# Performance work log

Measured on AMD Instinct MI355X. Metric: run time of the kernel, lower is better.

Reference implementation:

```python
import jax, jax.numpy as jnp
import numpy as np

B, S, N, D, H, M, P_OFF = 16, 4, 2048, 128, 16, 4096, 4092


def setup_inputs() -> dict:
    key = jax.random.key(0)
    ks = jax.random.split(key, 6)
    return {
        "X": jax.random.normal(ks[0], (B, S, N), dtype=jnp.float32),
        "W_q": jax.random.normal(ks[1], (N, N), dtype=jnp.float32) * 0.02,
        "W_k": jax.random.normal(ks[2], (N, N), dtype=jnp.float32) * 0.02,
        "W_v": jax.random.normal(ks[3], (N, N), dtype=jnp.float32) * 0.02,
        "cache_K": jax.random.normal(ks[4], (B, H, M, D), dtype=jnp.float32),
        "cache_V": jax.random.normal(ks[5], (B, H, M, D), dtype=jnp.float32),
        "P": P_OFF,
    }


def reference(X, W_q, W_k, W_v, cache_K, cache_V, P):
    b, s, n = X.shape
    _, h, m, d = cache_K.shape
    # RMSNorm (no eps, no learned scale, matching the source)
    variance = jnp.mean(X * X, axis=-1, keepdims=True)
    X_norm = X * jax.lax.rsqrt(variance)
    # QKV projections -> [b, h, s, d]
    Q = (X_norm @ W_q).reshape(b, s, h, d).transpose(0, 2, 1, 3)
    K = (X_norm @ W_k).reshape(b, s, h, d).transpose(0, 2, 1, 3)
    V = (X_norm @ W_v).reshape(b, s, h, d).transpose(0, 2, 1, 3)
    # KV-cache write at static offset P
    cK = cache_K.at[:, :, P:P + s, :].set(K)
    cV = cache_V.at[:, :, P:P + s, :].set(V)
    # Attention over full cache (note: source applies no 1/sqrt(d) scale)
    scores = jnp.einsum("bhsd,bhmd->bhsm", Q, cK)
    attn = jax.nn.softmax(scores, axis=-1)
    O = jnp.einsum("bhsm,bhmd->bhsd", attn, cV)
    return O.transpose(0, 2, 1, 3).reshape(b, s, n)
```

## Files before the change

### kernel.cpp

```cpp
#include <hip/hip_runtime.h>
#include <hip/hip_bf16.h>
#include <math.h>

#define NB 16
#define NS 4
#define NN 2048
#define ND 128
#define NH 16
#define NM 4096
#define NCHK 8
#define CHROWS 512
#define TROWS 32
#define NT 16
#define NKC 16

#define XN_OFF   0u
#define Q_OFF    131072u
#define K_OFF    262144u
#define V_OFF    393216u
#define OP_OFF   524288u
#define ML_OFF   1572864u
#define PART_OFF 1589248u

__global__ __launch_bounds__(256) void k_rmsnorm(const float* __restrict__ X,
                                                 float* __restrict__ ws) {
    const int row = blockIdx.x;
    const int tid = threadIdx.x;
    const float* xr = X + (size_t)row * NN;
    float4 a = *(const float4*)(xr + tid * 4);
    float4 b = *(const float4*)(xr + 1024 + tid * 4);
    float ss = a.x*a.x + a.y*a.y + a.z*a.z + a.w*a.w
             + b.x*b.x + b.y*b.y + b.z*b.z + b.w*b.w;
    #pragma unroll
    for (int off = 32; off; off >>= 1) ss += __shfl_xor(ss, off);
    __shared__ float ls[4];
    if ((tid & 63) == 0) ls[tid >> 6] = ss;
    __syncthreads();
    const float r = rsqrtf((ls[0] + ls[1] + ls[2] + ls[3]) * (1.0f / NN));
    float* o = ws + XN_OFF + (size_t)row * NN;
    *(float4*)(o + tid * 4)        = make_float4(a.x*r, a.y*r, a.z*r, a.w*r);
    *(float4*)(o + 1024 + tid * 4) = make_float4(b.x*r, b.y*r, b.z*r, b.w*r);
}

__global__ __launch_bounds__(256) void k_qkv(const float* __restrict__ Wq,
                                             const float* __restrict__ Wk,
                                             const float* __restrict__ Wv,
                                             float* __restrict__ ws) {
    __shared__ float xsT[64][68];
    __shared__ float wt[64][132];
    const int ct    = blockIdx.x;
    const int which = blockIdx.y;
    const int kc    = blockIdx.z;
    const float* __restrict__ W = (which == 0) ? Wq : (which == 1) ? Wk : Wv;
    const int tid = threadIdx.x;
    const int c0  = ct * 128;
    const int rg  = tid >> 5;
    const int cg  = tid & 31;
    const float* xn = ws + XN_OFF;

    float4 acc[8];
    #pragma unroll
    for (int i = 0; i < 8; i++) acc[i] = make_float4(0.f, 0.f, 0.f, 0.f);

    for (int s = 0; s < 2; s++) {
        const int k0 = kc * 128 + s * 64;
        __syncthreads();
        {
            const int r  = tid >> 2;
            const int q4 = tid & 3;
            #pragma unroll
            for (int i = 0; i < 4; i++) {
                const int f4 = q4 + i * 4;
                float4 v = *(const float4*)(xn + (size_t)r * NN + k0 + f4 * 4);
                xsT[f4 * 4 + 0][r] = v.x;
                xsT[f4 * 4 + 1][r] = v.y;
                xsT[f4 * 4 + 2][r] = v.z;
                xsT[f4 * 4 + 3][r] = v.w;
            }
        }
        {
            #pragma unroll
            for (int j8 = 0; j8 < 8; j8++) {
                const int kk  = j8 * 8 + (tid >> 5);
                const int f4c = tid & 31;
                float4 v = *(const float4*)(W + (size_t)(k0 + kk) * NN + c0 + f4c * 4);
                *(float4*)&wt[kk][f4c * 4] = v;
            }
        }
        __syncthreads();
        #pragma unroll 8
        for (int kk = 0; kk < 64; kk++) {
            const float4 x0 = *(const float4*)&xsT[kk][rg * 8];
            const float4 x1 = *(const float4*)&xsT[kk][rg * 8 + 4];
            const float4 w4 = *(const float4*)&wt[kk][cg * 4];
            acc[0].x += x0.x*w4.x; acc[0].y += x0.x*w4.y; acc[0].z += x0.x*w4.z; acc[0].w += x0.x*w4.w;
            acc[1].x += x0.y*w4.x; acc[1].y += x0.y*w4.y; acc[1].z += x0.y*w4.z; acc[1].w += x0.y*w4.w;
            acc[2].x += x0.z*w4.x; acc[2].y += x0.z*w4.y; acc[2].z += x0.z*w4.z; acc[2].w += x0.z*w4.w;
            acc[3].x += x0.w*w4.x; acc[3].y += x0.w*w4.y; acc[3].z += x0.w*w4.z; acc[3].w += x0.w*w4.w;
            acc[4].x += x1.x*w4.x; acc[4].y += x1.x*w4.y; acc[4].z += x1.x*w4.z; acc[4].w += x1.x*w4.w;
            acc[5].x += x1.y*w4.x; acc[5].y += x1.y*w4.y; acc[5].z += x1.y*w4.z; acc[5].w += x1.y*w4.w;
            acc[6].x += x1.z*w4.x; acc[6].y += x1.z*w4.y; acc[6].z += x1.z*w4.z; acc[6].w += x1.z*w4.w;
            acc[7].x += x1.w*w4.x; acc[7].y += x1.w*w4.y; acc[7].z += x1.w*w4.z; acc[7].w += x1.w*w4.w;
        }
    }
    float* po = ws + PART_OFF + (size_t)(kc * 3 + which) * 131072u;
    #pragma unroll
    for (int i = 0; i < 8; i++)
        *(float4*)(po + (size_t)(rg * 8 + i) * NN + c0 + cg * 4) = acc[i];
}

__global__ __launch_bounds__(256) void k_reduce(float* __restrict__ ws) {
    const int idx = blockIdx.x * 256 + threadIdx.x;
    const int which = idx >> 15;
    const int off   = idx & 32767;
    float4 s = make_float4(0.f, 0.f, 0.f, 0.f);
    #pragma unroll
    for (int kcc = 0; kcc < NKC; kcc++) {
        const float4 v = *(const float4*)(ws + PART_OFF
                         + (size_t)(kcc * 3 + which) * 131072u + (size_t)off * 4);
        s.x += v.x; s.y += v.y; s.z += v.z; s.w += v.w;
    }
    *(float4*)(ws + Q_OFF + (size_t)which * 131072u + (size_t)off * 4) = s;
}

__global__ __launch_bounds__(256) void k_attn(const float* __restrict__ cK,
                                              const float* __restrict__ cV,
                                              const int* __restrict__ Pp,
                                              float* __restrict__ ws) {
    const int ch = blockIdx.x, h = blockIdx.y, b = blockIdx.z;
    const int tid = threadIdx.x;
    const int wv = tid >> 6, lane = tid & 63;
    const int half = lane >> 5, r32 = lane & 31;
    const int P = *Pp;
    __shared__ float Ks[2][TROWS * 128];
    __shared__ float Vs[2][TROWS * 128];
    __shared__ float Qs[4][128] __attribute__((aligned(16)));
    __shared__ float ps[TROWS][4] __attribute__((aligned(16)));
    __shared__ float facs[4] __attribute__((aligned(16)));
    __shared__ float Ow[4][4][128];
    __shared__ float mls[4][2];

    if (tid < 128) {
        const int q = tid >> 5, d = (tid & 31) * 4;
        *(float4*)&Qs[q][d] =
            *(const float4*)(ws + Q_OFF + (size_t)(b * 4 + q) * NN + h * 128 + d);
    }

    const float* kbase = cK + (size_t)(b * NH + h) * NM * ND;
    const float* vbase = cV + (size_t)(b * NH + h) * NM * ND;
    const float* knew  = ws + K_OFF;
    const float* vnew  = ws + V_OFF;
    const int mb0 = ch * CHROWS;

    auto STAGE = [&](int tt, int bufi) {
        const int mb = mb0 + tt * TROWS;
        #pragma unroll
        for (int i = 0; i < 4; i++) {
            const int g0  = (wv * 4 + i) * 64;
            const int g   = g0 + lane;
            const int row = g >> 5;
            const int c4  = g & 31;
            const int csw = c4 ^ (row & 7);
            const int mrow = mb + row;
            const float* src = (mrow >= P && mrow < P + NS)
                ? knew + (size_t)(b * 4 + (mrow - P)) * NN + h * 128 + csw * 4
                : kbase + (size_t)mrow * ND + csw * 4;
            __builtin_amdgcn_global_load_lds(
                (const __attribute__((address_space(1))) void*)src,
                (__attribute__((address_space(3))) void*)(&Ks[bufi][g0 * 4]),
                16, 0, 0);
        }
        #pragma unroll
        for (int i = 0; i < 4; i++) {
            const int g0  = (wv * 4 + i) * 64;
            const int g   = g0 + lane;
            const int row = g >> 5;
            const int c4  = g & 31;
            const int mrow = mb + row;
            const float* src = (mrow >= P && mrow < P + NS)
                ? vnew + (size_t)(b * 4 + (mrow - P)) * NN + h * 128 + c4 * 4
                : vbase + (size_t)mrow * ND + c4 * 4;
            __builtin_amdgcn_global_load_lds(
                (const __attribute__((address_space(1))) void*)src,
                (__attribute__((address_space(3))) void*)(&Vs[bufi][g0 * 4]),
                16, 0, 0);
        }
    };

    float m_run = -INFINITY, l_run = 0.f;
    float2 Oa[4];
    #pragma unroll
    for (int q = 0; q < 4; q++) Oa[q] = make_float2(0.f, 0.f);

    STAGE(0, 0);
    __syncthreads();

    for (int t = 0; t < NT; t++) {
        const int cur = t & 1;
        if (t < NT - 1) STAGE(t + 1, cur ^ 1);

        const int s7 = r32 & 7;
        const float* kr = &Ks[cur][r32 * 128 + half * 64];
        const float* qr = &Qs[wv][half * 64];
        float s = 0.f;
        #pragma unroll
        for (int j = 0; j < 16; j++) {
            const float4 k4 = *(const float4*)&kr[(j ^ s7) * 4];
            const float4 q4 = *(const float4*)&qr[j * 4];
            s += k4.x*q4.x + k4.y*q4.y + k4.z*q4.z + k4.w*q4.w;
        }
        s += __shfl_xor(s, 32);
        float wm = s;
        #pragma unroll
        for (int off = 16; off; off >>= 1) wm = fmaxf(wm, __shfl_xor(wm, off));
        const float mn  = fmaxf(m_run, wm);
        const float fac = __expf(m_run - mn);
        m_run = mn;
        const float p = __expf(s - mn);
        l_run = l_run * fac + ((half == 0) ? p : 0.f);
        if (half == 0) ps[r32][wv] = p;
        if (lane == 0) facs[wv] = fac;
        asm volatile("s_waitcnt lgkmcnt(0)" ::: "memory");
        __builtin_amdgcn_s_barrier();
        __builtin_amdgcn_sched_barrier(0);

        const float4 fq = *(const float4*)&facs[0];
        Oa[0].x *= fq.x; Oa[0].y *= fq.x;
        Oa[1].x *= fq.y; Oa[1].y *= fq.y;
        Oa[2].x *= fq.z; Oa[2].y *= fq.z;
        Oa[3].x *= fq.w; Oa[3].y *= fq.w;
        const int r0 = wv * 8;
        #pragma unroll
        for (int rr = 0; rr < 8; rr++) {
            const float2 v2 = *(const float2*)&Vs[cur][(r0 + rr) * 128 + lane * 2];
            const float4 pr = *(const float4*)&ps[r0 + rr][0];
            Oa[0].x += pr.x * v2.x; Oa[0].y += pr.x * v2.y;
            Oa[1].x += pr.y * v2.x; Oa[1].y += pr.y * v2.y;
            Oa[2].x += pr.z * v2.x; Oa[2].y += pr.z * v2.y;
            Oa[3].x += pr.w * v2.x; Oa[3].y += pr.w * v2.y;
        }
        __syncthreads();
    }

    #pragma unroll
    for (int off = 32; off; off >>= 1) l_run += __shfl_xor(l_run, off);
    #pragma unroll
    for (int q = 0; q < 4; q++)
        *(float2*)&Ow[wv][q][lane * 2] = Oa[q];
    if (lane == 0) { mls[wv][0] = m_run; mls[wv][1] = l_run; }
    __syncthreads();

    const int q = wv;
    const int d0 = lane * 2;
    float o0 = 0.f, o1 = 0.f;
    #pragma unroll
    for (int w2 = 0; w2 < 4; w2++) {
        o0 += Ow[w2][q][d0];
        o1 += Ow[w2][q][d0 + 1];
    }
    const size_t bh = (size_t)(b * NH + h);
    const size_t pidx = ((bh * NCHK + ch) * 4 + q) * 128 + d0;
    ws[OP_OFF + pidx]     = o0;
    ws[OP_OFF + pidx + 1] = o1;
    if (lane == 0) {
        const size_t mi = ((bh * NCHK + ch) * 4 + q) * 2;
        ws[ML_OFF + mi]     = mls[q][0];
        ws[ML_OFF + mi + 1] = mls[q][1];
    }
}

__global__ __launch_bounds__(256) void k_comb(const float* __restrict__ ws,
                                              float* __restrict__ out) {
    const int bh = blockIdx.x;
    const int b = bh >> 4, h = bh & 15;
    const int tid = threadIdx.x;
    const int q = tid >> 6, d0 = (tid & 63) * 2;
    float ms = -INFINITY;
    #pragma unroll
    for (int c = 0; c < NCHK; c++)
        ms = fmaxf(ms, ws[ML_OFF + (((size_t)bh * NCHK + c) * 4 + q) * 2]);
    float o0 = 0.f, o1 = 0.f, den = 0.f;
    #pragma unroll
    for (int c = 0; c < NCHK; c++) {
        const size_t mi = (((size_t)bh * NCHK + c) * 4 + q) * 2;
        float e = __expf(ws[ML_OFF + mi] - ms);
        den += e * ws[ML_OFF + mi + 1];
        const size_t pi = (((size_t)bh * NCHK + c) * 4 + q) * 128 + d0;
        o0 += e * ws[OP_OFF + pi];
        o1 += e * ws[OP_OFF + pi + 1];
    }
    const float inv = 1.0f / den;
    const size_t oi = (size_t)(b * 4 + q) * NN + h * 128 + d0;
    *(float2*)(out + oi) = make_float2(o0 * inv, o1 * inv);
}

extern "C" void kernel_launch(void* const* d_in, const int* in_sizes, int n_in,
                              void* d_out, int out_size, void* d_ws, size_t ws_size,
                              hipStream_t stream) {
    const float* X  = (const float*)d_in[0];
    const float* Wq = (const float*)d_in[1];
    const float* Wk = (const float*)d_in[2];
    const float* Wv = (const float*)d_in[3];
    const float* cK = (const float*)d_in[4];
    const float* cV = (const float*)d_in[5];
    const int*   Pp = (const int*)d_in[6];
    float* ws = (float*)d_ws;
    float* out = (float*)d_out;

    hipLaunchKernelGGL(k_rmsnorm, dim3(64), dim3(256), 0, stream, X, ws);
    hipLaunchKernelGGL(k_qkv, dim3(16, 3, NKC), dim3(256), 0, stream, Wq, Wk, Wv, ws);
    hipLaunchKernelGGL(k_reduce, dim3(384), dim3(256), 0, stream, ws);
    hipLaunchKernelGGL(k_attn, dim3(NCHK, NH, NB), dim3(256), 0, stream, cK, cV, Pp, ws);
    hipLaunchKernelGGL(k_comb, dim3(NB * NH), dim3(256), 0, stream, ws, out);
}
```

Baseline: 238.2 us.

## Halve attention tile rows and fold RMSNorm scaling into QKV loads

```diff
diff --git a/kernel.cpp b/kernel.cpp
--- a/kernel.cpp
+++ b/kernel.cpp
@@ -10,11 +10,11 @@
 #define NM 4096
 #define NCHK 8
 #define CHROWS 512
-#define TROWS 32
-#define NT 16
+#define TROWS 16
+#define NT 32
 #define NKC 16
 
-#define XN_OFF   0u
+#define SC_OFF   0u
 #define Q_OFF    131072u
 #define K_OFF    262144u
 #define V_OFF    393216u
@@ -36,13 +36,12 @@
     __shared__ float ls[4];
     if ((tid & 63) == 0) ls[tid >> 6] = ss;
     __syncthreads();
-    const float r = rsqrtf((ls[0] + ls[1] + ls[2] + ls[3]) * (1.0f / NN));
-    float* o = ws + XN_OFF + (size_t)row * NN;
-    *(float4*)(o + tid * 4)        = make_float4(a.x*r, a.y*r, a.z*r, a.w*r);
-    *(float4*)(o + 1024 + tid * 4) = make_float4(b.x*r, b.y*r, b.z*r, b.w*r);
-}
-
-__global__ __launch_bounds__(256) void k_qkv(const float* __restrict__ Wq,
+    if (tid == 0)
+        ws[SC_OFF + row] = rsqrtf((ls[0] + ls[1] + ls[2] + ls[3]) * (1.0f / NN));
+}
+
+__global__ __launch_bounds__(256) void k_qkv(const float* __restrict__ X,
+                                             const float* __restrict__ Wq,
                                              const float* __restrict__ Wk,
                                              const float* __restrict__ Wv,
                                              float* __restrict__ ws) {
@@ -56,7 +55,7 @@
     const int c0  = ct * 128;
     const int rg  = tid >> 5;
     const int cg  = tid & 31;
-    const float* xn = ws + XN_OFF;
+    const float scl = ws[SC_OFF + (tid >> 2)];
 
     float4 acc[8];
     #pragma unroll
@@ -71,11 +70,11 @@
             #pragma unroll
             for (int i = 0; i < 4; i++) {
                 const int f4 = q4 + i * 4;
-                float4 v = *(const float4*)(xn + (size_t)r * NN + k0 + f4 * 4);
-                xsT[f4 * 4 + 0][r] = v.x;
-                xsT[f4 * 4 + 1][r] = v.y;
-                xsT[f4 * 4 + 2][r] = v.z;
-                xsT[f4 * 4 + 3][r] = v.w;
+                float4 v = *(const float4*)(X + (size_t)r * NN + k0 + f4 * 4);
+                xsT[f4 * 4 + 0][r] = v.x * scl;
+                xsT[f4 * 4 + 1][r] = v.y * scl;
+                xsT[f4 * 4 + 2][r] = v.z * scl;
+                xsT[f4 * 4 + 3][r] = v.w * scl;
             }
         }
         {
@@ -130,20 +129,21 @@
     const int ch = blockIdx.x, h = blockIdx.y, b = blockIdx.z;
     const int tid = threadIdx.x;
     const int wv = tid >> 6, lane = tid & 63;
-    const int half = lane >> 5, r32 = lane & 31;
+    const int r16 = lane & 15, qd = lane >> 4;
     const int P = *Pp;
     __shared__ float Ks[2][TROWS * 128];
     __shared__ float Vs[2][TROWS * 128];
-    __shared__ float Qs[4][128] __attribute__((aligned(16)));
+    __shared__ float Qs[4][4][40] __attribute__((aligned(16)));
     __shared__ float ps[TROWS][4] __attribute__((aligned(16)));
     __shared__ float facs[4] __attribute__((aligned(16)));
     __shared__ float Ow[4][4][128];
     __shared__ float mls[4][2];
 
     if (tid < 128) {
-        const int q = tid >> 5, d = (tid & 31) * 4;
-        *(float4*)&Qs[q][d] =
-            *(const float4*)(ws + Q_OFF + (size_t)(b * 4 + q) * NN + h * 128 + d);
+        const int q = tid >> 5, idx = tid & 31;
+        const int qq = idx >> 3, jj = idx & 7;
+        *(float4*)&Qs[q][qq][jj * 4] =
+            *(const float4*)(ws + Q_OFF + (size_t)(b * 4 + q) * NN + h * 128 + idx * 4);
     }
 
     const float* kbase = cK + (size_t)(b * NH + h) * NM * ND;
@@ -155,8 +155,8 @@
     auto STAGE = [&](int tt, int bufi) {
         const int mb = mb0 + tt * TROWS;
         #pragma unroll
-        for (int i = 0; i < 4; i++) {
-            const int g0  = (wv * 4 + i) * 64;
+        for (int i = 0; i < 2; i++) {
+            const int g0  = (wv * 2 + i) * 64;
             const int g   = g0 + lane;
             const int row = g >> 5;
             const int c4  = g & 31;
@@ -171,8 +171,8 @@
                 16, 0, 0);
         }
         #pragma unroll
-        for (int i = 0; i < 4; i++) {
-            const int g0  = (wv * 4 + i) * 64;
+        for (int i = 0; i < 2; i++) {
+            const int g0  = (wv * 2 + i) * 64;
             const int g   = g0 + lane;
             const int row = g >> 5;
             const int c4  = g & 31;
@@ -199,26 +199,27 @@
         const int cur = t & 1;
         if (t < NT - 1) STAGE(t + 1, cur ^ 1);
 
-        const int s7 = r32 & 7;
-        const float* kr = &Ks[cur][r32 * 128 + half * 64];
-        const float* qr = &Qs[wv][half * 64];
+        const int s7 = r16 & 7;
+        const float* kr = &Ks[cur][r16 * 128 + qd * 32];
+        const float* qr = &Qs[wv][qd][0];
         float s = 0.f;
         #pragma unroll
-        for (int j = 0; j < 16; j++) {
+        for (int j = 0; j < 8; j++) {
             const float4 k4 = *(const float4*)&kr[(j ^ s7) * 4];
             const float4 q4 = *(const float4*)&qr[j * 4];
             s += k4.x*q4.x + k4.y*q4.y + k4.z*q4.z + k4.w*q4.w;
         }
+        s += __shfl_xor(s, 16);
         s += __shfl_xor(s, 32);
         float wm = s;
         #pragma unroll
-        for (int off = 16; off; off >>= 1) wm = fmaxf(wm, __shfl_xor(wm, off));
+        for (int off = 8; off; off >>= 1) wm = fmaxf(wm, __shfl_xor(wm, off));
         const float mn  = fmaxf(m_run, wm);
         const float fac = __expf(m_run - mn);
         m_run = mn;
         const float p = __expf(s - mn);
-        l_run = l_run * fac + ((half == 0) ? p : 0.f);
-        if (half == 0) ps[r32][wv] = p;
+        l_run = l_run * fac + ((qd == 0) ? p : 0.f);
+        if (qd == 0) ps[r16][wv] = p;
         if (lane == 0) facs[wv] = fac;
         asm volatile("s_waitcnt lgkmcnt(0)" ::: "memory");
         __builtin_amdgcn_s_barrier();
@@ -229,9 +230,9 @@
         Oa[1].x *= fq.y; Oa[1].y *= fq.y;
         Oa[2].x *= fq.z; Oa[2].y *= fq.z;
         Oa[3].x *= fq.w; Oa[3].y *= fq.w;
-        const int r0 = wv * 8;
-        #pragma unroll
-        for (int rr = 0; rr < 8; rr++) {
+        const int r0 = wv * 4;
+        #pragma unroll
+        for (int rr = 0; rr < 4; rr++) {
             const float2 v2 = *(const float2*)&Vs[cur][(r0 + rr) * 128 + lane * 2];
             const float4 pr = *(const float4*)&ps[r0 + rr][0];
             Oa[0].x += pr.x * v2.x; Oa[0].y += pr.x * v2.y;
@@ -308,7 +309,7 @@
     float* out = (float*)d_out;
 
     hipLaunchKernelGGL(k_rmsnorm, dim3(64), dim3(256), 0, stream, X, ws);
-    hipLaunchKernelGGL(k_qkv, dim3(16, 3, NKC), dim3(256), 0, stream, Wq, Wk, Wv, ws);
+    hipLaunchKernelGGL(k_qkv, dim3(16, 3, NKC), dim3(256), 0, stream, X, Wq, Wk, Wv, ws);
     hipLaunchKernelGGL(k_reduce, dim3(384), dim3(256), 0, stream, ws);
     hipLaunchKernelGGL(k_attn, dim3(NCHK, NH, NB), dim3(256), 0, stream, cK, cV, Pp, ws);
     hipLaunchKernelGGL(k_comb, dim3(NB * NH), dim3(256), 0, stream, ws, out);
```

Result: slower. 247.7 us (+4.0%).

## Triple-buffer attention K/V staging and fold RMSNorm scale into QKV load

Applied to the files above, without the earlier changes.

```diff
diff --git a/kernel.cpp b/kernel.cpp
--- a/kernel.cpp
+++ b/kernel.cpp
@@ -14,7 +14,7 @@
 #define NT 16
 #define NKC 16
 
-#define XN_OFF   0u
+#define SC_OFF   0u
 #define Q_OFF    131072u
 #define K_OFF    262144u
 #define V_OFF    393216u
@@ -36,13 +36,12 @@
     __shared__ float ls[4];
     if ((tid & 63) == 0) ls[tid >> 6] = ss;
     __syncthreads();
-    const float r = rsqrtf((ls[0] + ls[1] + ls[2] + ls[3]) * (1.0f / NN));
-    float* o = ws + XN_OFF + (size_t)row * NN;
-    *(float4*)(o + tid * 4)        = make_float4(a.x*r, a.y*r, a.z*r, a.w*r);
-    *(float4*)(o + 1024 + tid * 4) = make_float4(b.x*r, b.y*r, b.z*r, b.w*r);
-}
-
-__global__ __launch_bounds__(256) void k_qkv(const float* __restrict__ Wq,
+    if (tid == 0)
+        ws[SC_OFF + row] = rsqrtf((ls[0] + ls[1] + ls[2] + ls[3]) * (1.0f / NN));
+}
+
+__global__ __launch_bounds__(256) void k_qkv(const float* __restrict__ X,
+                                             const float* __restrict__ Wq,
                                              const float* __restrict__ Wk,
                                              const float* __restrict__ Wv,
                                              float* __restrict__ ws) {
@@ -56,7 +55,7 @@
     const int c0  = ct * 128;
     const int rg  = tid >> 5;
     const int cg  = tid & 31;
-    const float* xn = ws + XN_OFF;
+    const float scl = ws[SC_OFF + (tid >> 2)];
 
     float4 acc[8];
     #pragma unroll
@@ -71,11 +70,11 @@
             #pragma unroll
             for (int i = 0; i < 4; i++) {
                 const int f4 = q4 + i * 4;
-                float4 v = *(const float4*)(xn + (size_t)r * NN + k0 + f4 * 4);
-                xsT[f4 * 4 + 0][r] = v.x;
-                xsT[f4 * 4 + 1][r] = v.y;
-                xsT[f4 * 4 + 2][r] = v.z;
-                xsT[f4 * 4 + 3][r] = v.w;
+                float4 v = *(const float4*)(X + (size_t)r * NN + k0 + f4 * 4);
+                xsT[f4 * 4 + 0][r] = v.x * scl;
+                xsT[f4 * 4 + 1][r] = v.y * scl;
+                xsT[f4 * 4 + 2][r] = v.z * scl;
+                xsT[f4 * 4 + 3][r] = v.w * scl;
             }
         }
         {
@@ -132,8 +131,8 @@
     const int wv = tid >> 6, lane = tid & 63;
     const int half = lane >> 5, r32 = lane & 31;
     const int P = *Pp;
-    __shared__ float Ks[2][TROWS * 128];
-    __shared__ float Vs[2][TROWS * 128];
+    __shared__ float Ks[3][TROWS * 128];
+    __shared__ float Vs[3][TROWS * 128];
     __shared__ float Qs[4][128] __attribute__((aligned(16)));
     __shared__ float ps[TROWS][4] __attribute__((aligned(16)));
     __shared__ float facs[4] __attribute__((aligned(16)));
@@ -193,11 +192,16 @@
     for (int q = 0; q < 4; q++) Oa[q] = make_float2(0.f, 0.f);
 
     STAGE(0, 0);
-    __syncthreads();
+    STAGE(1, 1);
 
     for (int t = 0; t < NT; t++) {
-        const int cur = t & 1;
-        if (t < NT - 1) STAGE(t + 1, cur ^ 1);
+        const int cur = t % 3;
+        if (t < NT - 1)
+            asm volatile("s_waitcnt vmcnt(8) lgkmcnt(0)" ::: "memory");
+        else
+            asm volatile("s_waitcnt vmcnt(0) lgkmcnt(0)" ::: "memory");
+        __builtin_amdgcn_s_barrier();
+        __builtin_amdgcn_sched_barrier(0);
 
         const int s7 = r32 & 7;
         const float* kr = &Ks[cur][r32 * 128 + half * 64];
@@ -220,6 +224,9 @@
         l_run = l_run * fac + ((half == 0) ? p : 0.f);
         if (half == 0) ps[r32][wv] = p;
         if (lane == 0) facs[wv] = fac;
+
+        if (t + 2 < NT) STAGE(t + 2, (t + 2) % 3);
+
         asm volatile("s_waitcnt lgkmcnt(0)" ::: "memory");
         __builtin_amdgcn_s_barrier();
         __builtin_amdgcn_sched_barrier(0);
@@ -239,7 +246,6 @@
             Oa[2].x += pr.z * v2.x; Oa[2].y += pr.z * v2.y;
             Oa[3].x += pr.w * v2.x; Oa[3].y += pr.w * v2.y;
         }
-        __syncthreads();
     }
 
     #pragma unroll
@@ -308,7 +314,7 @@
     float* out = (float*)d_out;
 
     hipLaunchKernelGGL(k_rmsnorm, dim3(64), dim3(256), 0, stream, X, ws);
-    hipLaunchKernelGGL(k_qkv, dim3(16, 3, NKC), dim3(256), 0, stream, Wq, Wk, Wv, ws);
+    hipLaunchKernelGGL(k_qkv, dim3(16, 3, NKC), dim3(256), 0, stream, X, Wq, Wk, Wv, ws);
     hipLaunchKernelGGL(k_reduce, dim3(384), dim3(256), 0, stream, ws);
     hipLaunchKernelGGL(k_attn, dim3(NCHK, NH, NB), dim3(256), 0, stream, cK, cV, Pp, ws);
     hipLaunchKernelGGL(k_comb, dim3(NB * NH), dim3(256), 0, stream, ws, out);
```

After: 331.0 us. 1.39x slower.
